# Kernel tuning notes

Measured on AMD Instinct MI355X. Metric: run time of the kernel, lower is better.

## Reference

```python
import jax, jax.numpy as jnp
import numpy as np

B, S, D_IN = 2, 2048, 1024
DIM, H, G = 64, 16, 4  # head dim, num_heads, kv groups


def setup_inputs() -> dict:
    key = jax.random.key(0)
    ks = jax.random.split(key, 9)
    query = jax.random.normal(ks[0], (B, S, D_IN), dtype=jnp.float32)
    key_t = jax.random.normal(ks[1], (B, S, D_IN), dtype=jnp.float32)
    value = jax.random.normal(ks[2], (B, S, D_IN), dtype=jnp.float32)
    # causal mask; masked_fill where mask == 0
    mask = jnp.tril(jnp.ones((S, S), dtype=jnp.int32))[None]  # [1,S,S]
    sc = 1.0 / np.sqrt(D_IN)
    Wq = jax.random.normal(ks[3], (H, D_IN, DIM), dtype=jnp.float32) * sc
    bq = jnp.zeros((H, DIM), dtype=jnp.float32)
    Wk = jax.random.normal(ks[4], (G, D_IN, DIM), dtype=jnp.float32) * sc
    bk = jnp.zeros((G, DIM), dtype=jnp.float32)
    Wv = jax.random.normal(ks[5], (G, D_IN, DIM), dtype=jnp.float32) * sc
    bv = jnp.zeros((G, DIM), dtype=jnp.float32)
    return {"query": query, "key": key_t, "value": value, "mask": mask,
            "Wq": Wq, "bq": bq, "Wk": Wk, "bk": bk, "Wv": Wv, "bv": bv}


def reference(query, key, value, mask, Wq, bq, Wk, bk, Wv, bv):
    # batched per-head projections (replaces the Python loop over heads)
    Q = jnp.einsum('bsd,hde->bhse', query, Wq) + bq[None, :, None, :]   # [B,H,S,E]
    K = jnp.einsum('bsd,gde->bgse', key, Wk) + bk[None, :, None, :]     # [B,G,S,E]
    V = jnp.einsum('bsd,gde->bgse', value, Wv) + bv[None, :, None, :]   # [B,G,S,E]
    # head i uses KV group i % G (as in the original loop)
    g_idx = jnp.arange(H) % G
    Kh = K[:, g_idx]  # [B,H,S,E]
    Vh = V[:, g_idx]
    attn = jnp.einsum('bhqe,bhke->bhqk', Q, Kh) / np.sqrt(DIM)          # [B,H,S,S]
    attn = jnp.where(mask[:, None] == 0, jnp.float32(-1e9), attn)
    p = jax.nn.softmax(attn, axis=-1)
    z = jnp.einsum('bhqk,bhke->bhqe', p, Vh)                             # [B,H,S,E]
    # concat heads along last dim (same order as torch.cat of z_list)
    return z.transpose(0, 2, 1, 3).reshape(B, S, H * DIM)
```

## Files before the change

### kernel.cpp

```cpp
#include <hip/hip_runtime.h>
#include <hip/hip_bf16.h>
#include <math.h>

#define S_LEN 2048
#define DIN   1024
#define NH    16
#define NG    4

typedef short s16x8 __attribute__((ext_vector_type(8)));
typedef float f32x4 __attribute__((ext_vector_type(4)));

__device__ __forceinline__ unsigned short f2bf(float x) {
  union { float f; unsigned u; } v; v.f = x;
  unsigned r = v.u + 0x7FFFu + ((v.u >> 16) & 1u);
  return (unsigned short)(r >> 16);
}
__device__ __forceinline__ unsigned cvtpk(float a, float b) {
  unsigned r;
  asm("v_cvt_pk_bf16_f32 %0, %1, %2" : "=v"(r) : "v"(a), "v"(b));
  return r;
}


__global__ __launch_bounds__(256) void k_cast(
    const float* __restrict__ q, const float* __restrict__ k,
    const float* __restrict__ v, unsigned short* __restrict__ AF) {
  const float* src = (blockIdx.y == 0) ? q : (blockIdx.y == 1) ? k : v;
  unsigned short* dst = AF + (size_t)blockIdx.y * 4194304;
  int flat = blockIdx.x * 256 + threadIdx.x;
  int b = flat >> 18, s = (flat >> 7) & 2047, d0 = (flat & 127) * 8;
  const float* sp = src + (size_t)(b * 2048 + s) * 1024 + d0;
  float4 x = *(const float4*)sp;
  float4 y = *(const float4*)(sp + 4);
  union { s16x8 v; unsigned u[4]; } r;
  r.u[0] = cvtpk(x.x, x.y); r.u[1] = cvtpk(x.z, x.w);
  r.u[2] = cvtpk(y.x, y.y); r.u[3] = cvtpk(y.z, y.w);
  unsigned short* p = dst + (size_t)((b * 128 + (s >> 4)) * 32 + (d0 >> 5)) * 512
                    + (s & 15) * 8 + ((d0 >> 3) & 3) * 128;
  *(s16x8*)p = r.v;
}

__global__ __launch_bounds__(256) void k_wtrans(
    const float* __restrict__ Wq, const float* __restrict__ Wk,
    const float* __restrict__ Wv, unsigned short* __restrict__ WF) {
  __shared__ __align__(16) unsigned short T[64][72];
  const int u = blockIdx.x >> 4, D0 = (blockIdx.x & 15) * 64;
  const int t = threadIdx.x;
  const float* src = (u < 16) ? (Wq + (size_t)u * 65536)
                   : (u < 20) ? (Wk + (size_t)(u - 16) * 65536)
                              : (Wv + (size_t)(u - 20) * 65536);
  const int e4 = (t & 15) * 4, dl = t >> 4;
  #pragma unroll
  for (int p = 0; p < 4; ++p) {
    const int d = p * 16 + dl;
    float4 v = *(const float4*)(src + (size_t)(D0 + d) * 64 + e4);
    T[e4 + 0][d] = f2bf(v.x); T[e4 + 1][d] = f2bf(v.y);
    T[e4 + 2][d] = f2bf(v.z); T[e4 + 3][d] = f2bf(v.w);
  }
  __syncthreads();
  const int j = t & 7;
  #pragma unroll
  for (int p = 0; p < 2; ++p) {
    const int e = p * 32 + (t >> 3);
    unsigned short* dst = WF + (size_t)u * 65536
        + (size_t)((e >> 4) * 32 + (D0 >> 5) + (j >> 2)) * 512
        + (e & 15) * 8 + (j & 3) * 128;
    *(s16x8*)dst = *(const s16x8*)&T[e][j * 8];
  }
}

__global__ __launch_bounds__(256, 2) void k_project(
    const unsigned short* __restrict__ AF,
    const float* __restrict__ bq, const float* __restrict__ bk,
    const float* __restrict__ bv,
    const unsigned short* __restrict__ WF,
    unsigned short* __restrict__ QF,
    unsigned short* __restrict__ KF,
    unsigned short* __restrict__ VF) {
  const int i = blockIdx.x;
  const int strip = i & 7, rr = i >> 3;
  const int b = rr / 24, u = rr % 24;
  const int tid = threadIdx.x;
  const int w = tid >> 6, lane = tid & 63, lq = lane & 15, gq = lane >> 4;

  const unsigned short* AFp = AF
      + (size_t)((u < 16) ? 0 : (u < 20) ? 1 : 2) * 4194304
      + (size_t)b * 2097152;
  const float* bias = (u < 16) ? bq + u * 64
                    : (u < 20) ? bk + (u - 16) * 64 : bv + (u - 20) * 64;
  const unsigned short* WFp = WF + (size_t)u * 65536;
  const int sb0 = strip * 16 + w * 4;

  f32x4 acc[4][4] = {};
  #pragma unroll 2
  for (int dk = 0; dk < 32; ++dk) {
    s16x8 a[4], bf[4];
    #pragma unroll
    for (int rf = 0; rf < 4; ++rf)
      a[rf] = *(const s16x8*)(AFp + (size_t)((sb0 + rf) * 32 + dk) * 512 + lane * 8);
    #pragma unroll
    for (int n = 0; n < 4; ++n)
      bf[n] = *(const s16x8*)(WFp + (size_t)(n * 32 + dk) * 512 + lane * 8);
    #pragma unroll
    for (int rf = 0; rf < 4; ++rf)
      #pragma unroll
      for (int n = 0; n < 4; ++n)
        acc[rf][n] = __builtin_amdgcn_mfma_f32_16x16x32_bf16(a[rf], bf[n], acc[rf][n], 0, 0, 0);
  }

  float bvv[4];
  #pragma unroll
  for (int n = 0; n < 4; ++n) bvv[n] = bias[n * 16 + lq];

  unsigned short* dst = (u < 16) ? QF + (size_t)(b * 16 + u) * 131072
                      : (u < 20) ? KF + (size_t)(b * 4 + (u - 16)) * 131072
                                 : VF + (size_t)(b * 4 + (u - 20)) * 131072;
  #pragma unroll
  for (int rf = 0; rf < 4; ++rf)
    #pragma unroll
    for (int n = 0; n < 4; ++n)
      #pragma unroll
      for (int r = 0; r < 4; ++r) {
        const int s = strip * 256 + w * 64 + rf * 16 + gq * 4 + r;
        const int d = n * 16 + lq;
        const unsigned short hv = f2bf(acc[rf][n][r] + bvv[n]);
        if (u < 20)
          dst[(size_t)((s >> 4) * 2 + (d >> 5)) * 512
              + (s & 15) * 8 + ((d >> 3) & 3) * 128 + (d & 7)] = hv;
        else
          dst[(size_t)(n * 64 + (s >> 5)) * 512
              + lq * 8 + ((s >> 3) & 3) * 128 + (s & 7)] = hv;
      }
}

__global__ __launch_bounds__(64, 2) void k_attn(
    const unsigned short* __restrict__ QF, const unsigned short* __restrict__ KF,
    const unsigned short* __restrict__ VF, float* __restrict__ out) {
  __shared__ __align__(16) unsigned short P[16][72];
  const int lane = threadIdx.x, lq = lane & 15, gq = lane >> 4;
  const int bidx = blockIdx.x;
  const int lid = (bidx & 7) * 128 + (bidx >> 3);
  const int pr = lid & 63, h = lid >> 6;
  const int b = blockIdx.y, g = h & 3;

  const unsigned short* QFp = QF + (size_t)(b * NH + h) * 131072;
  const unsigned short* KFp = KF + (size_t)(b * NG + g) * 131072;
  const unsigned short* VFp = VF + (size_t)(b * NG + g) * 131072;
  float* outp = out + (size_t)b * S_LEN * 1024 + h * 64;
  const float SC = 0.1803368801111204f;

  auto process = [&](int j) {
    const int ntiles = (j >> 2) + 1;
    const s16x8 qf0 = *(const s16x8*)(QFp + (size_t)(j * 2 + 0) * 512 + lane * 8);
    const s16x8 qf1 = *(const s16x8*)(QFp + (size_t)(j * 2 + 1) * 512 + lane * 8);
    f32x4 z[4] = {};
    float m = -INFINITY, l = 0.f;

    auto loadK = [&](s16x8 (&A)[4], s16x8 (&B)[4], int t) {
      #pragma unroll
      for (int f = 0; f < 4; ++f) {
        const unsigned short* kp = KFp + (size_t)((t * 4 + f) * 2) * 512 + lane * 8;
        A[f] = *(const s16x8*)kp;
        B[f] = *(const s16x8*)(kp + 512);
      }
    };

    auto tile = [&](const s16x8 (&kA)[4], const s16x8 (&kB)[4], int t) {
      const int k0 = t * 64;
      s16x8 vb[4][2];
      #pragma unroll
      for (int n = 0; n < 4; ++n)
        #pragma unroll
        for (int ks = 0; ks < 2; ++ks)
          vb[n][ks] = *(const s16x8*)(VFp + (size_t)(n * 64 + t * 2 + ks) * 512 + lane * 8);
      f32x4 sv[4];
      __builtin_amdgcn_s_setprio(1);
      #pragma unroll
      for (int f = 0; f < 4; ++f) {
        f32x4 s = {};
        s = __builtin_amdgcn_mfma_f32_16x16x32_bf16(kA[f], qf0, s, 0, 0, 0);
        s = __builtin_amdgcn_mfma_f32_16x16x32_bf16(kB[f], qf1, s, 0, 0, 0);
        sv[f] = s;
      }
      __builtin_amdgcn_s_setprio(0);
      #pragma unroll
      for (int f = 0; f < 4; ++f)
        #pragma unroll
        for (int r = 0; r < 4; ++r) sv[f][r] *= SC;
      if (t == ntiles - 1) {
        const int qrow = j * 16 + lq;
        #pragma unroll
        for (int f = 0; f < 4; ++f)
          #pragma unroll
          for (int r = 0; r < 4; ++r)
            if (k0 + f * 16 + gq * 4 + r > qrow) sv[f][r] = -1e30f;
      }
      float mf[4];
      #pragma unroll
      for (int f = 0; f < 4; ++f)
        mf[f] = fmaxf(fmaxf(sv[f][0], sv[f][1]), fmaxf(sv[f][2], sv[f][3]));
      float pm = fmaxf(fmaxf(mf[0], mf[1]), fmaxf(mf[2], mf[3]));
      pm = fmaxf(pm, __shfl_xor(pm, 16));
      pm = fmaxf(pm, __shfl_xor(pm, 32));
      if (__any(pm - m > 8.f)) {
        const float mn = fmaxf(m, pm);
        const float sc = __builtin_amdgcn_exp2f(m - mn);
        m = mn; l *= sc;
        #pragma unroll
        for (int r = 0; r < 4; ++r) {
          float scr = __shfl(sc, gq * 4 + r, 64);
          z[0][r] *= scr; z[1][r] *= scr; z[2][r] *= scr; z[3][r] *= scr;
        }
      }
      float s0 = 0.f, s1 = 0.f;
      #pragma unroll
      for (int f = 0; f < 4; ++f) {
        float p0 = __builtin_amdgcn_exp2f(sv[f][0] - m);
        float p1 = __builtin_amdgcn_exp2f(sv[f][1] - m);
        float p2 = __builtin_amdgcn_exp2f(sv[f][2] - m);
        float p3 = __builtin_amdgcn_exp2f(sv[f][3] - m);
        s0 += p0 + p1; s1 += p2 + p3;
        *(uint2*)&P[lq][f * 16 + gq * 4] = make_uint2(cvtpk(p0, p1), cvtpk(p2, p3));
      }
      float ss = s0 + s1;
      ss += __shfl_xor(ss, 16);
      ss += __shfl_xor(ss, 32);
      l += ss;
      s16x8 pa[2];
      #pragma unroll
      for (int ks = 0; ks < 2; ++ks)
        pa[ks] = *(const s16x8*)&P[lq][ks * 32 + gq * 8];
      __builtin_amdgcn_s_setprio(1);
      #pragma unroll
      for (int n = 0; n < 4; ++n)
        #pragma unroll
        for (int ks = 0; ks < 2; ++ks)
          z[n] = __builtin_amdgcn_mfma_f32_16x16x32_bf16(pa[ks], vb[n][ks], z[n], 0, 0, 0);
      __builtin_amdgcn_s_setprio(0);
    };

    s16x8 cA[4], cB[4], nA[4], nB[4];
    loadK(cA, cB, 0);
    int t = 0;
    while (true) {
      loadK(nA, nB, (t + 1 < ntiles) ? t + 1 : t);
      tile(cA, cB, t);
      if (++t >= ntiles) break;
      loadK(cA, cB, (t + 1 < ntiles) ? t + 1 : t);
      tile(nA, nB, t);
      if (++t >= ntiles) break;
    }

    #pragma unroll
    for (int r = 0; r < 4; ++r) {
      float lr = __shfl(l, gq * 4 + r, 64);
      float inv = __builtin_amdgcn_rcpf(lr);
      float* op = outp + (size_t)(j * 16 + gq * 4 + r) * 1024;
      #pragma unroll
      for (int n = 0; n < 4; ++n) op[n * 16 + lq] = z[n][r] * inv;
    }
  };

  process(pr);
  process(127 - pr);
}

extern "C" void kernel_launch(void* const* d_in, const int* in_sizes, int n_in,
                              void* d_out, int out_size, void* d_ws, size_t ws_size,
                              hipStream_t stream) {
  const float* query = (const float*)d_in[0];
  const float* key   = (const float*)d_in[1];
  const float* value = (const float*)d_in[2];
  const float* Wq = (const float*)d_in[4];
  const float* bq = (const float*)d_in[5];
  const float* Wk = (const float*)d_in[6];
  const float* bk = (const float*)d_in[7];
  const float* Wv = (const float*)d_in[8];
  const float* bv = (const float*)d_in[9];
  float* out = (float*)d_out;

  unsigned short* AF = (unsigned short*)d_ws;
  unsigned short* WF = AF + 12582912;
  unsigned short* QF = WF + 1572864;
  unsigned short* KF = QF + 4194304;
  unsigned short* VF = KF + 1048576;

  hipLaunchKernelGGL(k_cast, dim3(2048, 3), dim3(256), 0, stream,
                     query, key, value, AF);
  hipLaunchKernelGGL(k_wtrans, dim3(384), dim3(256), 0, stream, Wq, Wk, Wv, WF);
  hipLaunchKernelGGL(k_project, dim3(384), dim3(256), 0, stream,
                     AF, bq, bk, bv, WF, QF, KF, VF);
  hipLaunchKernelGGL(k_attn, dim3(1024, 2), dim3(64), 0, stream, QF, KF, VF, out);
}
```

Measured before the change: 100.8 us.

## Fuse input cast into projection and split attention KV tiles across two waves

Drops the separate fp32-to-bf16 cast kernel. The projection GEMM now loads fp32 activations directly and converts them in registers, using smaller per-wave row tiles over twice as many blocks. The attention kernel now gives each query block to two waves that take alternate KV tiles, then merges their softmax states through shared memory. This replaces the earlier pairing of query blocks to balance the causal workload. The aim is to remove a full intermediate write and read and to add parallelism to attention, at the cost of uncoalesced fp32 A loads in the GEMM and a block-level sync and merge step.

```diff
diff --git a/kernel.cpp b/kernel.cpp
--- a/kernel.cpp
+++ b/kernel.cpp
@@ -20,25 +20,13 @@
   asm("v_cvt_pk_bf16_f32 %0, %1, %2" : "=v"(r) : "v"(a), "v"(b));
   return r;
 }
-
-
-__global__ __launch_bounds__(256) void k_cast(
-    const float* __restrict__ q, const float* __restrict__ k,
-    const float* __restrict__ v, unsigned short* __restrict__ AF) {
-  const float* src = (blockIdx.y == 0) ? q : (blockIdx.y == 1) ? k : v;
-  unsigned short* dst = AF + (size_t)blockIdx.y * 4194304;
-  int flat = blockIdx.x * 256 + threadIdx.x;
-  int b = flat >> 18, s = (flat >> 7) & 2047, d0 = (flat & 127) * 8;
-  const float* sp = src + (size_t)(b * 2048 + s) * 1024 + d0;
-  float4 x = *(const float4*)sp;
-  float4 y = *(const float4*)(sp + 4);
+__device__ __forceinline__ s16x8 cvt8(float4 a, float4 b) {
   union { s16x8 v; unsigned u[4]; } r;
-  r.u[0] = cvtpk(x.x, x.y); r.u[1] = cvtpk(x.z, x.w);
-  r.u[2] = cvtpk(y.x, y.y); r.u[3] = cvtpk(y.z, y.w);
-  unsigned short* p = dst + (size_t)((b * 128 + (s >> 4)) * 32 + (d0 >> 5)) * 512
-                    + (s & 15) * 8 + ((d0 >> 3) & 3) * 128;
-  *(s16x8*)p = r.v;
-}
+  r.u[0] = cvtpk(a.x, a.y); r.u[1] = cvtpk(a.z, a.w);
+  r.u[2] = cvtpk(b.x, b.y); r.u[3] = cvtpk(b.z, b.w);
+  return r.v;
+}
+
 
 __global__ __launch_bounds__(256) void k_wtrans(
     const float* __restrict__ Wq, const float* __restrict__ Wk,
@@ -70,7 +58,8 @@
 }
 
 __global__ __launch_bounds__(256, 2) void k_project(
-    const unsigned short* __restrict__ AF,
+    const float* __restrict__ query, const float* __restrict__ key,
+    const float* __restrict__ value,
     const float* __restrict__ bq, const float* __restrict__ bk,
     const float* __restrict__ bv,
     const unsigned short* __restrict__ WF,
@@ -78,31 +67,35 @@
     unsigned short* __restrict__ KF,
     unsigned short* __restrict__ VF) {
   const int i = blockIdx.x;
-  const int strip = i & 7, rr = i >> 3;
+  const int lid = (i & 7) * 96 + (i >> 3);
+  const int strip = lid / 48;
+  const int rr = lid % 48;
   const int b = rr / 24, u = rr % 24;
   const int tid = threadIdx.x;
   const int w = tid >> 6, lane = tid & 63, lq = lane & 15, gq = lane >> 4;
-
-  const unsigned short* AFp = AF
-      + (size_t)((u < 16) ? 0 : (u < 20) ? 1 : 2) * 4194304
-      + (size_t)b * 2097152;
-  const float* bias = (u < 16) ? bq + u * 64
-                    : (u < 20) ? bk + (u - 16) * 64 : bv + (u - 20) * 64;
+  const int row0 = strip * 128 + w * 32;
+
+  const float* src; const float* bias;
+  if (u < 16)      { src = query; bias = bq + u * 64; }
+  else if (u < 20) { src = key;   bias = bk + (u - 16) * 64; }
+  else             { src = value; bias = bv + (u - 20) * 64; }
+  src += (size_t)b * S_LEN * DIN;
   const unsigned short* WFp = WF + (size_t)u * 65536;
-  const int sb0 = strip * 16 + w * 4;
-
-  f32x4 acc[4][4] = {};
+
+  f32x4 acc[2][4] = {};
   #pragma unroll 2
   for (int dk = 0; dk < 32; ++dk) {
-    s16x8 a[4], bf[4];
-    #pragma unroll
-    for (int rf = 0; rf < 4; ++rf)
-      a[rf] = *(const s16x8*)(AFp + (size_t)((sb0 + rf) * 32 + dk) * 512 + lane * 8);
+    s16x8 a[2], bf[4];
+    #pragma unroll
+    for (int rf = 0; rf < 2; ++rf) {
+      const float* ap = src + (size_t)(row0 + rf * 16 + lq) * DIN + dk * 32 + gq * 8;
+      a[rf] = cvt8(*(const float4*)ap, *(const float4*)(ap + 4));
+    }
     #pragma unroll
     for (int n = 0; n < 4; ++n)
       bf[n] = *(const s16x8*)(WFp + (size_t)(n * 32 + dk) * 512 + lane * 8);
     #pragma unroll
-    for (int rf = 0; rf < 4; ++rf)
+    for (int rf = 0; rf < 2; ++rf)
       #pragma unroll
       for (int n = 0; n < 4; ++n)
         acc[rf][n] = __builtin_amdgcn_mfma_f32_16x16x32_bf16(a[rf], bf[n], acc[rf][n], 0, 0, 0);
@@ -116,12 +109,12 @@
                       : (u < 20) ? KF + (size_t)(b * 4 + (u - 16)) * 131072
                                  : VF + (size_t)(b * 4 + (u - 20)) * 131072;
   #pragma unroll
-  for (int rf = 0; rf < 4; ++rf)
+  for (int rf = 0; rf < 2; ++rf)
     #pragma unroll
     for (int n = 0; n < 4; ++n)
       #pragma unroll
       for (int r = 0; r < 4; ++r) {
-        const int s = strip * 256 + w * 64 + rf * 16 + gq * 4 + r;
+        const int s = row0 + rf * 16 + gq * 4 + r;
         const int d = n * 16 + lq;
         const unsigned short hv = f2bf(acc[rf][n][r] + bvv[n]);
         if (u < 20)
@@ -133,136 +126,155 @@
       }
 }
 
-__global__ __launch_bounds__(64, 2) void k_attn(
+__global__ __launch_bounds__(128) void k_attn(
     const unsigned short* __restrict__ QF, const unsigned short* __restrict__ KF,
     const unsigned short* __restrict__ VF, float* __restrict__ out) {
-  __shared__ __align__(16) unsigned short P[16][72];
-  const int lane = threadIdx.x, lq = lane & 15, gq = lane >> 4;
-  const int bidx = blockIdx.x;
-  const int lid = (bidx & 7) * 128 + (bidx >> 3);
-  const int pr = lid & 63, h = lid >> 6;
+  __shared__ __align__(16) unsigned short P[2][16][72];
+  __shared__ float CMz[64][17];
+  __shared__ float CMml[64][2];
+  const int tid = threadIdx.x;
+  const int w = tid >> 6, lane = tid & 63, lq = lane & 15, gq = lane >> 4;
+  const int x = blockIdx.x;
+  const int lid = (x & 7) * 256 + (x >> 3);
+  const int j = lid & 127, h = lid >> 7;
   const int b = blockIdx.y, g = h & 3;
 
   const unsigned short* QFp = QF + (size_t)(b * NH + h) * 131072;
   const unsigned short* KFp = KF + (size_t)(b * NG + g) * 131072;
   const unsigned short* VFp = VF + (size_t)(b * NG + g) * 131072;
-  float* outp = out + (size_t)b * S_LEN * 1024 + h * 64;
   const float SC = 0.1803368801111204f;
-
-  auto process = [&](int j) {
-    const int ntiles = (j >> 2) + 1;
-    const s16x8 qf0 = *(const s16x8*)(QFp + (size_t)(j * 2 + 0) * 512 + lane * 8);
-    const s16x8 qf1 = *(const s16x8*)(QFp + (size_t)(j * 2 + 1) * 512 + lane * 8);
-    f32x4 z[4] = {};
-    float m = -INFINITY, l = 0.f;
-
-    auto loadK = [&](s16x8 (&A)[4], s16x8 (&B)[4], int t) {
-      #pragma unroll
-      for (int f = 0; f < 4; ++f) {
-        const unsigned short* kp = KFp + (size_t)((t * 4 + f) * 2) * 512 + lane * 8;
-        A[f] = *(const s16x8*)kp;
-        B[f] = *(const s16x8*)(kp + 512);
-      }
-    };
-
-    auto tile = [&](const s16x8 (&kA)[4], const s16x8 (&kB)[4], int t) {
-      const int k0 = t * 64;
-      s16x8 vb[4][2];
-      #pragma unroll
-      for (int n = 0; n < 4; ++n)
-        #pragma unroll
-        for (int ks = 0; ks < 2; ++ks)
-          vb[n][ks] = *(const s16x8*)(VFp + (size_t)(n * 64 + t * 2 + ks) * 512 + lane * 8);
-      f32x4 sv[4];
-      __builtin_amdgcn_s_setprio(1);
-      #pragma unroll
-      for (int f = 0; f < 4; ++f) {
-        f32x4 s = {};
-        s = __builtin_amdgcn_mfma_f32_16x16x32_bf16(kA[f], qf0, s, 0, 0, 0);
-        s = __builtin_amdgcn_mfma_f32_16x16x32_bf16(kB[f], qf1, s, 0, 0, 0);
-        sv[f] = s;
-      }
-      __builtin_amdgcn_s_setprio(0);
+  const int nt = (j >> 2) + 1;
+
+  const s16x8 qf0 = *(const s16x8*)(QFp + (size_t)(j * 2 + 0) * 512 + lane * 8);
+  const s16x8 qf1 = *(const s16x8*)(QFp + (size_t)(j * 2 + 1) * 512 + lane * 8);
+  f32x4 z[4] = {};
+  float m = -INFINITY, l = 0.f;
+
+  auto loadK = [&](s16x8 (&A)[4], s16x8 (&B)[4], int t) {
+    #pragma unroll
+    for (int f = 0; f < 4; ++f) {
+      const unsigned short* kp = KFp + (size_t)((t * 4 + f) * 2) * 512 + lane * 8;
+      A[f] = *(const s16x8*)kp;
+      B[f] = *(const s16x8*)(kp + 512);
+    }
+  };
+
+  auto tile = [&](const s16x8 (&kA)[4], const s16x8 (&kB)[4], int t) {
+    const int k0 = t * 64;
+    s16x8 vb[4][2];
+    #pragma unroll
+    for (int n = 0; n < 4; ++n)
+      #pragma unroll
+      for (int ks = 0; ks < 2; ++ks)
+        vb[n][ks] = *(const s16x8*)(VFp + (size_t)(n * 64 + t * 2 + ks) * 512 + lane * 8);
+    f32x4 sv[4];
+    __builtin_amdgcn_s_setprio(1);
+    #pragma unroll
+    for (int f = 0; f < 4; ++f) {
+      f32x4 s = {};
+      s = __builtin_amdgcn_mfma_f32_16x16x32_bf16(kA[f], qf0, s, 0, 0, 0);
+      s = __builtin_amdgcn_mfma_f32_16x16x32_bf16(kB[f], qf1, s, 0, 0, 0);
+      sv[f] = s;
+    }
+    __builtin_amdgcn_s_setprio(0);
+    #pragma unroll
+    for (int f = 0; f < 4; ++f)
+      #pragma unroll
+      for (int r = 0; r < 4; ++r) sv[f][r] *= SC;
+    if (t == nt - 1) {
+      const int qrow = j * 16 + lq;
       #pragma unroll
       for (int f = 0; f < 4; ++f)
         #pragma unroll
-        for (int r = 0; r < 4; ++r) sv[f][r] *= SC;
-      if (t == ntiles - 1) {
-        const int qrow = j * 16 + lq;
-        #pragma unroll
-        for (int f = 0; f < 4; ++f)
-          #pragma unroll
-          for (int r = 0; r < 4; ++r)
-            if (k0 + f * 16 + gq * 4 + r > qrow) sv[f][r] = -1e30f;
+        for (int r = 0; r < 4; ++r)
+          if (k0 + f * 16 + gq * 4 + r > qrow) sv[f][r] = -1e30f;
+    }
+    float mf[4];
+    #pragma unroll
+    for (int f = 0; f < 4; ++f)
+      mf[f] = fmaxf(fmaxf(sv[f][0], sv[f][1]), fmaxf(sv[f][2], sv[f][3]));
+    float pm = fmaxf(fmaxf(mf[0], mf[1]), fmaxf(mf[2], mf[3]));
+    pm = fmaxf(pm, __shfl_xor(pm, 16));
+    pm = fmaxf(pm, __shfl_xor(pm, 32));
+    if (__any(pm - m > 8.f)) {
+      const float mn = fmaxf(m, pm);
+      const float sc = __builtin_amdgcn_exp2f(m - mn);
+      m = mn; l *= sc;
+      #pragma unroll
+      for (int r = 0; r < 4; ++r) {
+        float scr = __shfl(sc, gq * 4 + r, 64);
+        z[0][r] *= scr; z[1][r] *= scr; z[2][r] *= scr; z[3][r] *= scr;
       }
-      float mf[4];
-      #pragma unroll
-      for (int f = 0; f < 4; ++f)
-        mf[f] = fmaxf(fmaxf(sv[f][0], sv[f][1]), fmaxf(sv[f][2], sv[f][3]));
-      float pm = fmaxf(fmaxf(mf[0], mf[1]), fmaxf(mf[2], mf[3]));
-      pm = fmaxf(pm, __shfl_xor(pm, 16));
-      pm = fmaxf(pm, __shfl_xor(pm, 32));
-      if (__any(pm - m > 8.f)) {
-        const float mn = fmaxf(m, pm);
-        const float sc = __builtin_amdgcn_exp2f(m - mn);
-        m = mn; l *= sc;
-        #pragma unroll
-        for (int r = 0; r < 4; ++r) {
-          float scr = __shfl(sc, gq * 4 + r, 64);
-          z[0][r] *= scr; z[1][r] *= scr; z[2][r] *= scr; z[3][r] *= scr;
-        }
-      }
-      float s0 = 0.f, s1 = 0.f;
-      #pragma unroll
-      for (int f = 0; f < 4; ++f) {
-        float p0 = __builtin_amdgcn_exp2f(sv[f][0] - m);
-        float p1 = __builtin_amdgcn_exp2f(sv[f][1] - m);
-        float p2 = __builtin_amdgcn_exp2f(sv[f][2] - m);
-        float p3 = __builtin_amdgcn_exp2f(sv[f][3] - m);
-        s0 += p0 + p1; s1 += p2 + p3;
-        *(uint2*)&P[lq][f * 16 + gq * 4] = make_uint2(cvtpk(p0, p1), cvtpk(p2, p3));
-      }
-      float ss = s0 + s1;
-      ss += __shfl_xor(ss, 16);
-      ss += __shfl_xor(ss, 32);
-      l += ss;
-      s16x8 pa[2];
+    }
+    float s0 = 0.f, s1 = 0.f;
+    #pragma unroll
+    for (int f = 0; f < 4; ++f) {
+      float p0 = __builtin_amdgcn_exp2f(sv[f][0] - m);
+      float p1 = __builtin_amdgcn_exp2f(sv[f][1] - m);
+      float p2 = __builtin_amdgcn_exp2f(sv[f][2] - m);
+      float p3 = __builtin_amdgcn_exp2f(sv[f][3] - m);
+      s0 += p0 + p1; s1 += p2 + p3;
+      *(uint2*)&P[w][lq][f * 16 + gq * 4] = make_uint2(cvtpk(p0, p1), cvtpk(p2, p3));
+    }
+    float ss = s0 + s1;
+    ss += __shfl_xor(ss, 16);
+    ss += __shfl_xor(ss, 32);
+    l += ss;
+    s16x8 pa[2];
+    #pragma unroll
+    for (int ks = 0; ks < 2; ++ks)
+      pa[ks] = *(const s16x8*)&P[w][lq][ks * 32 + gq * 8];
+    __builtin_amdgcn_s_setprio(1);
+    #pragma unroll
+    for (int n = 0; n < 4; ++n)
       #pragma unroll
       for (int ks = 0; ks < 2; ++ks)
-        pa[ks] = *(const s16x8*)&P[lq][ks * 32 + gq * 8];
-      __builtin_amdgcn_s_setprio(1);
+        z[n] = __builtin_amdgcn_mfma_f32_16x16x32_bf16(pa[ks], vb[n][ks], z[n], 0, 0, 0);
+    __builtin_amdgcn_s_setprio(0);
+  };
+
+  int t = w;
+  if (t < nt) {
+    s16x8 cA[4], cB[4], nA[4], nB[4];
+    loadK(cA, cB, t);
+    while (true) {
+      loadK(nA, nB, (t + 2 < nt) ? t + 2 : t);
+      tile(cA, cB, t);
+      t += 2; if (t >= nt) break;
+      loadK(cA, cB, (t + 2 < nt) ? t + 2 : t);
+      tile(nA, nB, t);
+      t += 2; if (t >= nt) break;
+    }
+  }
+
+  if (w == 1) {
+    #pragma unroll
+    for (int n = 0; n < 4; ++n)
+      #pragma unroll
+      for (int r = 0; r < 4; ++r)
+        CMz[lane][n * 4 + r] = z[n][r];
+    CMml[lane][0] = m; CMml[lane][1] = l;
+  }
+  __syncthreads();
+  if (w == 0) {
+    const float m1 = CMml[lane][0], l1 = CMml[lane][1];
+    const float ms = fmaxf(m, m1);
+    const float a0 = __builtin_amdgcn_exp2f(m - ms);
+    const float a1 = __builtin_amdgcn_exp2f(m1 - ms);
+    const float lf = l * a0 + l1 * a1;
+    float* outp = out + (size_t)b * S_LEN * 1024 + h * 64;
+    #pragma unroll
+    for (int r = 0; r < 4; ++r) {
+      const float a0r = __shfl(a0, gq * 4 + r, 64);
+      const float a1r = __shfl(a1, gq * 4 + r, 64);
+      const float lr  = __shfl(lf, gq * 4 + r, 64);
+      const float inv = __builtin_amdgcn_rcpf(lr);
+      float* op = outp + (size_t)(j * 16 + gq * 4 + r) * 1024;
       #pragma unroll
       for (int n = 0; n < 4; ++n)
-        #pragma unroll
-        for (int ks = 0; ks < 2; ++ks)
-          z[n] = __builtin_amdgcn_mfma_f32_16x16x32_bf16(pa[ks], vb[n][ks], z[n], 0, 0, 0);
-      __builtin_amdgcn_s_setprio(0);
-    };
-
-    s16x8 cA[4], cB[4], nA[4], nB[4];
-    loadK(cA, cB, 0);
-    int t = 0;
-    while (true) {
-      loadK(nA, nB, (t + 1 < ntiles) ? t + 1 : t);
-      tile(cA, cB, t);
-      if (++t >= ntiles) break;
-      loadK(cA, cB, (t + 1 < ntiles) ? t + 1 : t);
-      tile(nA, nB, t);
-      if (++t >= ntiles) break;
-    }
-
-    #pragma unroll
-    for (int r = 0; r < 4; ++r) {
-      float lr = __shfl(l, gq * 4 + r, 64);
-      float inv = __builtin_amdgcn_rcpf(lr);
-      float* op = outp + (size_t)(j * 16 + gq * 4 + r) * 1024;
-      #pragma unroll
-      for (int n = 0; n < 4; ++n) op[n * 16 + lq] = z[n][r] * inv;
-    }
-  };
-
-  process(pr);
-  process(127 - pr);
+        op[n * 16 + lq] = (z[n][r] * a0r + CMz[lane][n * 4 + r] * a1r) * inv;
+    }
+  }
 }
 
 extern "C" void kernel_launch(void* const* d_in, const int* in_sizes, int n_in,
@@ -279,16 +291,13 @@
   const float* bv = (const float*)d_in[9];
   float* out = (float*)d_out;
 
-  unsigned short* AF = (unsigned short*)d_ws;
-  unsigned short* WF = AF + 12582912;
+  unsigned short* WF = (unsigned short*)d_ws;
   unsigned short* QF = WF + 1572864;
   unsigned short* KF = QF + 4194304;
   unsigned short* VF = KF + 1048576;
 
-  hipLaunchKernelGGL(k_cast, dim3(2048, 3), dim3(256), 0, stream,
-                     query, key, value, AF);
   hipLaunchKernelGGL(k_wtrans, dim3(384), dim3(256), 0, stream, Wq, Wk, Wv, WF);
-  hipLaunchKernelGGL(k_project, dim3(384), dim3(256), 0, stream,
-                     AF, bq, bk, bv, WF, QF, KF, VF);
-  hipLaunchKernelGGL(k_attn, dim3(1024, 2), dim3(64), 0, stream, QF, KF, VF, out);
-}
+  hipLaunchKernelGGL(k_project, dim3(768), dim3(256), 0, stream,
+                     query, key, value, bq, bk, bv, WF, QF, KF, VF);
+  hipLaunchKernelGGL(k_attn, dim3(2048, 2), dim3(128), 0, stream, QF, KF, VF, out);
+}
```

Measured after the change: 118.9 us. 18.0% more time.
